# Optimization experiments

Hardware: AMD Instinct MI355X
Metric: run time of the kernel (lower is better)

## Reference

```python
import jax, jax.numpy as jnp
import numpy as np


def setup_inputs() -> dict:
    key = jax.random.key(0)
    k1, k2 = jax.random.split(key)
    B, T, D, N = 8, 1024, 256, 8192
    x = jax.random.normal(k1, (B, T, D), dtype=jnp.float32)
    # codebook (kaiming-uniform in torch; gaussian stand-in, same math downstream)
    embed = jax.random.normal(k2, (N, D), dtype=jnp.float32)
    return {"x": x, "embed": embed}


def reference(x, embed):
    # encode: squared-Euclidean distances (argmin-equivalent to torch.cdist)
    x_sq = jnp.sum(x * x, axis=-1, keepdims=True)          # [B,T,1]
    e_sq = jnp.sum(embed * embed, axis=-1)                 # [N]
    xe = jnp.einsum('btd,nd->btn', x, embed)               # [B,T,N]
    dist2 = x_sq - 2.0 * xe + e_sq                         # [B,T,N]
    embed_ind = jnp.argmin(dist2, axis=-1)                 # [B,T] int
    # decode: embedding gather
    quantized = jnp.take(embed, embed_ind, axis=0)         # [B,T,D]
    return quantized, embed_ind
```

## Files before the change

kernel.cpp:

```cpp
#include <hip/hip_runtime.h>
#include <hip/hip_fp16.h>

typedef __attribute__((ext_vector_type(8))) _Float16 f16x8;
typedef __attribute__((ext_vector_type(16))) float f32x16;

#define M_TOT 8192
#define N_TOT 8192
#define K_TOT 256

__device__ __forceinline__ void load_lds16(const void* g, void* l) {
  __builtin_amdgcn_global_load_lds(
      (const __attribute__((address_space(1))) unsigned int*)g,
      (__attribute__((address_space(3))) unsigned int*)l, 16, 0, 0);
}
__device__ __forceinline__ double shfl_xor_d(double v, int m) {
  unsigned long long u = (unsigned long long)__double_as_longlong(v);
  unsigned lo = (unsigned)u, hi = (unsigned)(u >> 32);
  lo = __shfl_xor(lo, m, 64);
  hi = __shfl_xor(hi, m, 64);
  return __longlong_as_double((long long)((((unsigned long long)hi) << 32) | lo));
}

__global__ __launch_bounds__(256) void prep_kernel(
    const float* __restrict__ x, const float* __restrict__ embed,
    unsigned short* __restrict__ X0p, unsigned short* __restrict__ E0p,
    float* __restrict__ xsq, float* __restrict__ esq) {
  const int bid = blockIdx.x;
  const bool is_e = bid >= 2048;
  const int lb = is_e ? bid - 2048 : bid;
  const int t = lb * 256 + threadIdx.x;
  const float* __restrict__ in = is_e ? embed : x;
  unsigned short* __restrict__ p0 = is_e ? E0p : X0p;
  float* __restrict__ sq = is_e ? esq : xsq;

  float4 v = reinterpret_cast<const float4*>(in)[t];
  float f[4] = {v.x, v.y, v.z, v.w};
  unsigned short h[4];
#pragma unroll
  for (int c = 0; c < 4; ++c) h[c] = __half_as_ushort(__float2half_rn(f[c]));
  ushort4 o = {h[0], h[1], h[2], h[3]};
  reinterpret_cast<ushort4*>(p0)[t] = o;

  const int lane = threadIdx.x & 63;
  float s = f[0] * f[0] + f[1] * f[1] + f[2] * f[2] + f[3] * f[3];
#pragma unroll
  for (int off = 32; off > 0; off >>= 1) s += __shfl_xor(s, off, 64);
  if (lane == 0) sq[lb * 4 + (threadIdx.x >> 6)] = s;
}

__global__ __launch_bounds__(256, 3) void mfma_pmin_kernel(
    const unsigned short* __restrict__ X0p, const unsigned short* __restrict__ E0p,
    const float* __restrict__ esq, unsigned short* __restrict__ pmin) {
  __shared__ unsigned short lds[16384];

  const int tid = threadIdx.x;
  const int wid = tid >> 6;
  const int lane = tid & 63;
  const int li = lane & 15;
  const int lh = (lane >> 4) & 1;
  const int lq2 = lane >> 5;

  const int bid = blockIdx.x;
  const int nb = (bid & 7) * 8 + ((bid >> 3) & 7);
  const int mb = bid >> 6;
  const int m0 = mb * 128, n0 = nb * 128;
  const int wn = (wid >> 1) * 64, wm = (wid & 1) * 64;

  const int r_st = lane >> 2;
  const int kp_st = ((lane & 3) - (r_st >> 1)) & 3;
  const int sw_k0 = (li * 4 + ((lq2 + (li >> 1)) & 3)) * 8;
  const int sw_k1 = (li * 4 + ((2 + lq2 + (li >> 1)) & 3)) * 8;

  f32x16 acc[2][2];
#pragma unroll
  for (int a = 0; a < 2; ++a)
#pragma unroll
    for (int b = 0; b < 2; ++b)
#pragma unroll
      for (int r = 0; r < 16; ++r) acc[a][b][r] = 0.0f;

  const int eseg = (wn >> 4) + lh;
  const int xseg = (wm >> 4) + lh;

  for (int kc = 0; kc < 4; ++kc) {
    const int k0 = kc * 64;
    __syncthreads();
#pragma unroll
    for (int j = 0; j < 8; ++j) {
      const int tt = j * 4 + wid;
      const int tsel = tt >> 4;
      const int u = tt & 15;
      const int ksl = u >> 3, seg = u & 7;
      const int rowbase = (tsel ? m0 : n0) + seg * 16 + r_st;
      const unsigned short* src = tsel ? X0p : E0p;
      load_lds16(src + (size_t)rowbase * K_TOT + k0 + ksl * 32 + kp_st * 8,
                 &lds[tsel * 8192 + ksl * 4096 + seg * 512]);
    }
    __syncthreads();

#pragma unroll
    for (int ksl = 0; ksl < 2; ++ksl) {
      const unsigned short* Eb = &lds[ksl * 4096];
      const unsigned short* Xb = &lds[8192 + ksl * 4096];
      f16x8 ef[2][2];
#pragma unroll
      for (int et = 0; et < 2; ++et) {
        const unsigned short* eb = Eb + (eseg + et * 2) * 512;
        ef[et][0] = *(const f16x8*)(eb + sw_k0);
        ef[et][1] = *(const f16x8*)(eb + sw_k1);
      }
#pragma unroll
      for (int xt = 0; xt < 2; ++xt) {
        const unsigned short* xb = Xb + (xseg + xt * 2) * 512;
        f16x8 xf0 = *(const f16x8*)(xb + sw_k0);
        f16x8 xf1 = *(const f16x8*)(xb + sw_k1);
#pragma unroll
        for (int et = 0; et < 2; ++et) {
          f32x16 c = acc[et][xt];
          c = __builtin_amdgcn_mfma_f32_32x32x16_f16(ef[et][0], xf0, c, 0, 0, 0);
          c = __builtin_amdgcn_mfma_f32_32x32x16_f16(ef[et][1], xf1, c, 0, 0, 0);
          acc[et][xt] = c;
        }
      }
    }
  }

  float es[2][16];
#pragma unroll
  for (int et = 0; et < 2; ++et)
#pragma unroll
    for (int r = 0; r < 16; ++r)
      es[et][r] = esq[n0 + wn + et * 32 + (r & 3) + 8 * (r >> 2) + 4 * lq2];

#pragma unroll
  for (int xt = 0; xt < 2; ++xt) {
    unsigned short outv[4];
#pragma unroll
    for (int et = 0; et < 2; ++et) {
#pragma unroll
      for (int cell = 0; cell < 2; ++cell) {
        float mval = 3.4e38f;
#pragma unroll
        for (int rr = 0; rr < 8; ++rr) {
          const int r = cell * 8 + rr;
          mval = fminf(mval, es[et][r] - 2.0f * acc[et][xt][r]);
        }
        mval = fminf(mval, __shfl_xor(mval, 32, 64));
        outv[et * 2 + cell] = __half_as_ushort(__float2half_rd(mval));
      }
    }
    if (lq2 == 0) {
      const int xrow = m0 + wm + xt * 32 + (lane & 31);
      *reinterpret_cast<ushort4*>(&pmin[(size_t)xrow * 512 + ((n0 + wn) >> 4)]) =
          *reinterpret_cast<ushort4*>(outv);
    }
  }
}

__global__ __launch_bounds__(256) void refine_gather_kernel(
    const float* __restrict__ x, const float* __restrict__ embed,
    const float* __restrict__ xsq, const unsigned short* __restrict__ pmin,
    float* __restrict__ out) {
  const int row = blockIdx.x * 4 + (threadIdx.x >> 6);
  const int lane = threadIdx.x & 63;

  const unsigned short* pm = pmin + (size_t)row * 512 + lane * 8;
  int4 raw = *reinterpret_cast<const int4*>(pm);
  unsigned short cu[8];
  *reinterpret_cast<int4*>(cu) = raw;
  float cv[8];
#pragma unroll
  for (int j = 0; j < 8; ++j) cv[j] = __half2float(__ushort_as_half(cu[j]));
  float lm = cv[0];
#pragma unroll
  for (int j = 1; j < 8; ++j) lm = fminf(lm, cv[j]);
#pragma unroll
  for (int off = 1; off < 64; off <<= 1) lm = fminf(lm, __shfl_xor(lm, off, 64));

  const float thr = lm + sqrtf(xsq[row]) * (96.0f / 1024.0f) + 1.2f;

  const int c = lane & 15, q = lane >> 4;
  const float* xp = x + (size_t)row * K_TOT + q * 64;

  double bd = 1e300;
  int bidx = 1 << 30;
#pragma unroll
  for (int j = 0; j < 8; ++j) {
    unsigned long long mask = __ballot(cv[j] < thr);
    while (mask) {
      const int b = __ffsll((long long)mask) - 1;
      mask &= mask - 1;
      const int cell = b * 8 + j;
      const int col = cell * 16 + c;
      const float* ep = embed + (size_t)col * K_TOT + q * 64;
      double dd = 0.0;
#pragma unroll
      for (int i = 0; i < 16; ++i) {
        float4 e4 = reinterpret_cast<const float4*>(ep)[i];
        float4 x4 = reinterpret_cast<const float4*>(xp)[i];
        double d0 = (double)x4.x - (double)e4.x;
        double d1 = (double)x4.y - (double)e4.y;
        double d2 = (double)x4.z - (double)e4.z;
        double d3 = (double)x4.w - (double)e4.w;
        dd += d0 * d0 + d1 * d1 + d2 * d2 + d3 * d3;
      }
      dd += shfl_xor_d(dd, 16);
      dd += shfl_xor_d(dd, 32);
      int ci = col;
#pragma unroll
      for (int off = 1; off < 16; off <<= 1) {
        double od = shfl_xor_d(dd, off);
        int oi = __shfl_xor(ci, off, 64);
        if (od < dd || (od == dd && oi < ci)) { dd = od; ci = oi; }
      }
      if (dd < bd || (dd == bd && ci < bidx)) { bd = dd; bidx = ci; }
    }
  }

  reinterpret_cast<float4*>(out)[(size_t)row * 64 + lane] =
      reinterpret_cast<const float4*>(embed)[(size_t)bidx * 64 + lane];
  if (lane == 0) out[(size_t)M_TOT * K_TOT + row] = (float)bidx;
}

#define BM 32
#define BN 64
#define KC 32
#define NQ 2
#define NPQ (N_TOT / NQ)
#define SB 72

__global__ __launch_bounds__(256) void esq_kernel(const float* __restrict__ embed,
                                                  float* __restrict__ esq) {
  const int lane = threadIdx.x & 63;
  const int wave = threadIdx.x >> 6;
  const int code = blockIdx.x * 4 + wave;
  float4 v = reinterpret_cast<const float4*>(embed + (size_t)code * K_TOT)[lane];
  float s = v.x * v.x + v.y * v.y + v.z * v.z + v.w * v.w;
#pragma unroll
  for (int off = 32; off > 0; off >>= 1) s += __shfl_xor(s, off, 64);
  if (lane == 0) esq[code] = s;
}

__global__ __launch_bounds__(256, 2) void argmin_kernel(
    const float* __restrict__ x, const float* __restrict__ embed,
    const float* __restrict__ esq, float* __restrict__ pval, int* __restrict__ pidx) {
  __shared__ float A[K_TOT][BM];
  __shared__ float Bs[KC][SB];
  const int tid = threadIdx.x;
  const int tx = tid & 15;
  const int ty = tid >> 4;
  const int q = blockIdx.x & 1;
  const int mb = blockIdx.x >> 1;
  const int m0 = mb * BM;
  const int nq0 = q * NPQ;
#pragma unroll
  for (int it = 0; it < 8; ++it) {
    int idx = it * 256 + tid;
    int row = idx >> 6;
    int k4 = idx & 63;
    float4 v = reinterpret_cast<const float4*>(x + (size_t)(m0 + row) * K_TOT)[k4];
    A[k4 * 4 + 0][row] = v.x; A[k4 * 4 + 1][row] = v.y;
    A[k4 * 4 + 2][row] = v.z; A[k4 * 4 + 3][row] = v.w;
  }
  float minv[2]; int mini[2];
#pragma unroll
  for (int r = 0; r < 2; ++r) { minv[r] = 3.4e38f; mini[r] = 0; }
  for (int ns = 0; ns < NPQ / BN; ++ns) {
    const int n0 = nq0 + ns * BN;
    float acc[2][4];
#pragma unroll
    for (int r = 0; r < 2; ++r)
#pragma unroll
      for (int c = 0; c < 4; ++c) acc[r][c] = 0.0f;
    for (int kc = 0; kc < K_TOT / KC; ++kc) {
      const int k0 = kc * KC;
      __syncthreads();
#pragma unroll
      for (int it = 0; it < 2; ++it) {
        int idx = it * 256 + tid;
        int nl = idx >> 3;
        int k4 = idx & 7;
        float4 v = reinterpret_cast<const float4*>(embed + (size_t)(n0 + nl) * K_TOT + k0)[k4];
        Bs[k4 * 4 + 0][nl] = v.x; Bs[k4 * 4 + 1][nl] = v.y;
        Bs[k4 * 4 + 2][nl] = v.z; Bs[k4 * 4 + 3][nl] = v.w;
      }
      __syncthreads();
#pragma unroll
      for (int kk = 0; kk < KC; ++kk) {
        float2 a = *reinterpret_cast<const float2*>(&A[k0 + kk][ty * 2]);
        float4 b = *reinterpret_cast<const float4*>(&Bs[kk][tx * 4]);
        acc[0][0] += a.x * b.x; acc[0][1] += a.x * b.y;
        acc[0][2] += a.x * b.z; acc[0][3] += a.x * b.w;
        acc[1][0] += a.y * b.x; acc[1][1] += a.y * b.y;
        acc[1][2] += a.y * b.z; acc[1][3] += a.y * b.w;
      }
    }
    float4 es = *reinterpret_cast<const float4*>(&esq[n0 + tx * 4]);
    float e[4] = {es.x, es.y, es.z, es.w};
#pragma unroll
    for (int r = 0; r < 2; ++r)
#pragma unroll
      for (int c = 0; c < 4; ++c) {
        float d = e[c] - 2.0f * acc[r][c];
        int id = n0 + tx * 4 + c;
        if (d < minv[r]) { minv[r] = d; mini[r] = id; }
      }
  }
#pragma unroll
  for (int r = 0; r < 2; ++r) {
    float v = minv[r]; int i = mini[r];
#pragma unroll
    for (int off = 1; off < 16; off <<= 1) {
      float vo = __shfl_xor(v, off, 64);
      int io = __shfl_xor(i, off, 64);
      if (vo < v || (vo == v && io < i)) { v = vo; i = io; }
    }
    if (tx == 0) {
      int row = m0 + ty * 2 + r;
      pval[q * M_TOT + row] = v;
      pidx[q * M_TOT + row] = i;
    }
  }
}

__global__ __launch_bounds__(256) void gather_kernel(
    const float* __restrict__ embed, const float* __restrict__ pval,
    const int* __restrict__ pidx, float* __restrict__ out) {
  const int row = blockIdx.x;
  float bv = pval[row]; int bi = pidx[row];
#pragma unroll
  for (int qq = 1; qq < NQ; ++qq) {
    float v = pval[qq * M_TOT + row];
    int i = pidx[qq * M_TOT + row];
    if (v < bv || (v == bv && i < bi)) { bv = v; bi = i; }
  }
  out[(size_t)row * K_TOT + threadIdx.x] = embed[(size_t)bi * K_TOT + threadIdx.x];
  if (threadIdx.x == 0) out[(size_t)M_TOT * K_TOT + row] = (float)bi;
}

extern "C" void kernel_launch(void* const* d_in, const int* in_sizes, int n_in,
                              void* d_out, int out_size, void* d_ws, size_t ws_size,
                              hipStream_t stream) {
  const float* x = (const float*)d_in[0];
  const float* embed = (const float*)d_in[1];
  float* out = (float*)d_out;
  char* ws = (char*)d_ws;

  const size_t HALF_BYTES = (size_t)M_TOT * K_TOT * 2;
  const size_t PMIN_BYTES = (size_t)M_TOT * 512 * 2;
  const size_t need = (1u << 20) + 2 * HALF_BYTES + PMIN_BYTES;

  if (ws_size >= need) {
    float* xsq = (float*)ws;
    float* esq = (float*)(ws + 32768);
    unsigned short* X0p = (unsigned short*)(ws + (1u << 20));
    unsigned short* E0p = (unsigned short*)(ws + (1u << 20) + HALF_BYTES);
    unsigned short* pmin = (unsigned short*)(ws + (1u << 20) + 2 * HALF_BYTES);
    prep_kernel<<<4096, 256, 0, stream>>>(x, embed, X0p, E0p, xsq, esq);
    mfma_pmin_kernel<<<4096, 256, 0, stream>>>(X0p, E0p, esq, pmin);
    refine_gather_kernel<<<2048, 256, 0, stream>>>(x, embed, xsq, pmin, out);
  } else {
    float* esq = (float*)ws;
    float* pval = (float*)(ws + 32768);
    int* pidx = (int*)(ws + 32768 + NQ * 32768);
    esq_kernel<<<2048, 256, 0, stream>>>(embed, esq);
    argmin_kernel<<<512, 256, 0, stream>>>(x, embed, esq, pval, pidx);
    gather_kernel<<<M_TOT, 256, 0, stream>>>(embed, pval, pidx, out);
  }
}
```

Baseline: 150.6 us.

## Fuse prep, MFMA pmin and refine kernels into one persistent kernel with grid barriers

Merges the three launches into a single persistent kernel of 768 blocks that loops over work items in each phase. The phases are separated by a software grid barrier built on atomics, which removes the launch gaps and tail effects between kernels. The cost is barrier spin overhead and a hipMemsetAsync to reset the counter. It also relies on all 768 blocks being co-resident (3 per CU), and it will deadlock if they are not.

```diff
diff --git a/kernel.cpp b/kernel.cpp
--- a/kernel.cpp
+++ b/kernel.cpp
@@ -7,6 +7,7 @@
 #define M_TOT 8192
 #define N_TOT 8192
 #define K_TOT 256
+#define NBLK 768
 
 __device__ __forceinline__ void load_lds16(const void* g, void* l) {
   __builtin_amdgcn_global_load_lds(
@@ -21,205 +22,215 @@
   return __longlong_as_double((long long)((((unsigned long long)hi) << 32) | lo));
 }
 
-__global__ __launch_bounds__(256) void prep_kernel(
+__device__ __forceinline__ void grid_bar(unsigned* cnt, unsigned* sense, unsigned gen) {
+  __syncthreads();
+  if (threadIdx.x == 0) {
+    __threadfence();
+    unsigned arrived =
+        __hip_atomic_fetch_add(cnt, 1u, __ATOMIC_ACQ_REL, __HIP_MEMORY_SCOPE_AGENT) + 1;
+    if (arrived == gen * NBLK) {
+      __hip_atomic_store(sense, gen, __ATOMIC_RELEASE, __HIP_MEMORY_SCOPE_AGENT);
+    } else {
+      while (__hip_atomic_load(sense, __ATOMIC_ACQUIRE, __HIP_MEMORY_SCOPE_AGENT) < gen) {
+      }
+    }
+    __threadfence();
+  }
+  __syncthreads();
+}
+
+__global__ __launch_bounds__(256, 3) void fused_kernel(
     const float* __restrict__ x, const float* __restrict__ embed,
     unsigned short* __restrict__ X0p, unsigned short* __restrict__ E0p,
-    float* __restrict__ xsq, float* __restrict__ esq) {
-  const int bid = blockIdx.x;
-  const bool is_e = bid >= 2048;
-  const int lb = is_e ? bid - 2048 : bid;
-  const int t = lb * 256 + threadIdx.x;
-  const float* __restrict__ in = is_e ? embed : x;
-  unsigned short* __restrict__ p0 = is_e ? E0p : X0p;
-  float* __restrict__ sq = is_e ? esq : xsq;
-
-  float4 v = reinterpret_cast<const float4*>(in)[t];
-  float f[4] = {v.x, v.y, v.z, v.w};
-  unsigned short h[4];
-#pragma unroll
-  for (int c = 0; c < 4; ++c) h[c] = __half_as_ushort(__float2half_rn(f[c]));
-  ushort4 o = {h[0], h[1], h[2], h[3]};
-  reinterpret_cast<ushort4*>(p0)[t] = o;
-
-  const int lane = threadIdx.x & 63;
-  float s = f[0] * f[0] + f[1] * f[1] + f[2] * f[2] + f[3] * f[3];
-#pragma unroll
-  for (int off = 32; off > 0; off >>= 1) s += __shfl_xor(s, off, 64);
-  if (lane == 0) sq[lb * 4 + (threadIdx.x >> 6)] = s;
-}
-
-__global__ __launch_bounds__(256, 3) void mfma_pmin_kernel(
-    const unsigned short* __restrict__ X0p, const unsigned short* __restrict__ E0p,
-    const float* __restrict__ esq, unsigned short* __restrict__ pmin) {
+    float* __restrict__ xsq, float* __restrict__ esq,
+    unsigned short* __restrict__ pmin, unsigned* __restrict__ bar,
+    float* __restrict__ out) {
   __shared__ unsigned short lds[16384];
 
   const int tid = threadIdx.x;
   const int wid = tid >> 6;
   const int lane = tid & 63;
+
+  for (int rw = blockIdx.x * 4 + wid; rw < 16384; rw += NBLK * 4) {
+    const bool is_e = rw >= 8192;
+    const int row = rw & 8191;
+    const float* __restrict__ in = is_e ? embed : x;
+    unsigned short* __restrict__ p0 = is_e ? E0p : X0p;
+    float4 v = reinterpret_cast<const float4*>(in + (size_t)row * K_TOT)[lane];
+    float f[4] = {v.x, v.y, v.z, v.w};
+    unsigned short h[4];
+#pragma unroll
+    for (int c = 0; c < 4; ++c) h[c] = __half_as_ushort(__float2half_rn(f[c]));
+    ushort4 o = {h[0], h[1], h[2], h[3]};
+    reinterpret_cast<ushort4*>(p0 + (size_t)row * K_TOT)[lane] = o;
+    float s = f[0] * f[0] + f[1] * f[1] + f[2] * f[2] + f[3] * f[3];
+#pragma unroll
+    for (int off = 32; off > 0; off >>= 1) s += __shfl_xor(s, off, 64);
+    if (lane == 0) (is_e ? esq : xsq)[row] = s;
+  }
+
+  grid_bar(bar, bar + 1, 1);
+
   const int li = lane & 15;
   const int lh = (lane >> 4) & 1;
   const int lq2 = lane >> 5;
-
-  const int bid = blockIdx.x;
-  const int nb = (bid & 7) * 8 + ((bid >> 3) & 7);
-  const int mb = bid >> 6;
-  const int m0 = mb * 128, n0 = nb * 128;
-  const int wn = (wid >> 1) * 64, wm = (wid & 1) * 64;
-
   const int r_st = lane >> 2;
   const int kp_st = ((lane & 3) - (r_st >> 1)) & 3;
   const int sw_k0 = (li * 4 + ((lq2 + (li >> 1)) & 3)) * 8;
   const int sw_k1 = (li * 4 + ((2 + lq2 + (li >> 1)) & 3)) * 8;
 
-  f32x16 acc[2][2];
-#pragma unroll
-  for (int a = 0; a < 2; ++a)
-#pragma unroll
-    for (int b = 0; b < 2; ++b)
-#pragma unroll
-      for (int r = 0; r < 16; ++r) acc[a][b][r] = 0.0f;
-
-  const int eseg = (wn >> 4) + lh;
-  const int xseg = (wm >> 4) + lh;
-
-  for (int kc = 0; kc < 4; ++kc) {
-    const int k0 = kc * 64;
-    __syncthreads();
+  for (int t = blockIdx.x; t < 4096; t += NBLK) {
+    const int nb = (t & 7) * 8 + ((t >> 3) & 7);
+    const int mb = t >> 6;
+    const int m0 = mb * 128, n0 = nb * 128;
+    const int wn = (wid >> 1) * 64, wm = (wid & 1) * 64;
+
+    f32x16 acc[2][2];
+#pragma unroll
+    for (int a = 0; a < 2; ++a)
+#pragma unroll
+      for (int b = 0; b < 2; ++b)
+#pragma unroll
+        for (int r = 0; r < 16; ++r) acc[a][b][r] = 0.0f;
+
+    const int eseg = (wn >> 4) + lh;
+    const int xseg = (wm >> 4) + lh;
+
+    for (int kc = 0; kc < 4; ++kc) {
+      const int k0 = kc * 64;
+      __syncthreads();
+#pragma unroll
+      for (int j = 0; j < 8; ++j) {
+        const int tt = j * 4 + wid;
+        const int tsel = tt >> 4;
+        const int u = tt & 15;
+        const int ksl = u >> 3, seg = u & 7;
+        const int rowbase = (tsel ? m0 : n0) + seg * 16 + r_st;
+        const unsigned short* src = tsel ? X0p : E0p;
+        load_lds16(src + (size_t)rowbase * K_TOT + k0 + ksl * 32 + kp_st * 8,
+                   &lds[tsel * 8192 + ksl * 4096 + seg * 512]);
+      }
+      __syncthreads();
+
+#pragma unroll
+      for (int ksl = 0; ksl < 2; ++ksl) {
+        const unsigned short* Eb = &lds[ksl * 4096];
+        const unsigned short* Xb = &lds[8192 + ksl * 4096];
+        f16x8 ef[2][2];
+#pragma unroll
+        for (int et = 0; et < 2; ++et) {
+          const unsigned short* eb = Eb + (eseg + et * 2) * 512;
+          ef[et][0] = *(const f16x8*)(eb + sw_k0);
+          ef[et][1] = *(const f16x8*)(eb + sw_k1);
+        }
+#pragma unroll
+        for (int xt = 0; xt < 2; ++xt) {
+          const unsigned short* xb = Xb + (xseg + xt * 2) * 512;
+          f16x8 xf0 = *(const f16x8*)(xb + sw_k0);
+          f16x8 xf1 = *(const f16x8*)(xb + sw_k1);
+#pragma unroll
+          for (int et = 0; et < 2; ++et) {
+            f32x16 c = acc[et][xt];
+            c = __builtin_amdgcn_mfma_f32_32x32x16_f16(ef[et][0], xf0, c, 0, 0, 0);
+            c = __builtin_amdgcn_mfma_f32_32x32x16_f16(ef[et][1], xf1, c, 0, 0, 0);
+            acc[et][xt] = c;
+          }
+        }
+      }
+    }
+
+    float es[2][16];
+#pragma unroll
+    for (int et = 0; et < 2; ++et)
+#pragma unroll
+      for (int r = 0; r < 16; ++r)
+        es[et][r] = esq[n0 + wn + et * 32 + (r & 3) + 8 * (r >> 2) + 4 * lq2];
+
+#pragma unroll
+    for (int xt = 0; xt < 2; ++xt) {
+      unsigned short outv[4];
+#pragma unroll
+      for (int et = 0; et < 2; ++et) {
+#pragma unroll
+        for (int cell = 0; cell < 2; ++cell) {
+          float mval = 3.4e38f;
+#pragma unroll
+          for (int rr = 0; rr < 8; ++rr) {
+            const int r = cell * 8 + rr;
+            mval = fminf(mval, es[et][r] - 2.0f * acc[et][xt][r]);
+          }
+          mval = fminf(mval, __shfl_xor(mval, 32, 64));
+          outv[et * 2 + cell] = __half_as_ushort(__float2half_rd(mval));
+        }
+      }
+      if (lq2 == 0) {
+        const int xrow = m0 + wm + xt * 32 + (lane & 31);
+        *reinterpret_cast<ushort4*>(&pmin[(size_t)xrow * 512 + ((n0 + wn) >> 4)]) =
+            *reinterpret_cast<ushort4*>(outv);
+      }
+    }
+  }
+
+  grid_bar(bar, bar + 1, 2);
+
+  for (int row = blockIdx.x * 4 + wid; row < 8192; row += NBLK * 4) {
+    const unsigned short* pm = pmin + (size_t)row * 512 + lane * 8;
+    int4 raw = *reinterpret_cast<const int4*>(pm);
+    unsigned short cu[8];
+    *reinterpret_cast<int4*>(cu) = raw;
+    float cv[8];
+#pragma unroll
+    for (int j = 0; j < 8; ++j) cv[j] = __half2float(__ushort_as_half(cu[j]));
+    float lm = cv[0];
+#pragma unroll
+    for (int j = 1; j < 8; ++j) lm = fminf(lm, cv[j]);
+#pragma unroll
+    for (int off = 1; off < 64; off <<= 1) lm = fminf(lm, __shfl_xor(lm, off, 64));
+
+    const float thr = lm + sqrtf(xsq[row]) * (96.0f / 1024.0f) + 1.2f;
+
+    const int c = lane & 15, q = lane >> 4;
+    const float* xp = x + (size_t)row * K_TOT + q * 64;
+
+    double bd = 1e300;
+    int bidx = 1 << 30;
 #pragma unroll
     for (int j = 0; j < 8; ++j) {
-      const int tt = j * 4 + wid;
-      const int tsel = tt >> 4;
-      const int u = tt & 15;
-      const int ksl = u >> 3, seg = u & 7;
-      const int rowbase = (tsel ? m0 : n0) + seg * 16 + r_st;
-      const unsigned short* src = tsel ? X0p : E0p;
-      load_lds16(src + (size_t)rowbase * K_TOT + k0 + ksl * 32 + kp_st * 8,
-                 &lds[tsel * 8192 + ksl * 4096 + seg * 512]);
-    }
-    __syncthreads();
-
-#pragma unroll
-    for (int ksl = 0; ksl < 2; ++ksl) {
-      const unsigned short* Eb = &lds[ksl * 4096];
-      const unsigned short* Xb = &lds[8192 + ksl * 4096];
-      f16x8 ef[2][2];
-#pragma unroll
-      for (int et = 0; et < 2; ++et) {
-        const unsigned short* eb = Eb + (eseg + et * 2) * 512;
-        ef[et][0] = *(const f16x8*)(eb + sw_k0);
-        ef[et][1] = *(const f16x8*)(eb + sw_k1);
-      }
-#pragma unroll
-      for (int xt = 0; xt < 2; ++xt) {
-        const unsigned short* xb = Xb + (xseg + xt * 2) * 512;
-        f16x8 xf0 = *(const f16x8*)(xb + sw_k0);
-        f16x8 xf1 = *(const f16x8*)(xb + sw_k1);
-#pragma unroll
-        for (int et = 0; et < 2; ++et) {
-          f32x16 c = acc[et][xt];
-          c = __builtin_amdgcn_mfma_f32_32x32x16_f16(ef[et][0], xf0, c, 0, 0, 0);
-          c = __builtin_amdgcn_mfma_f32_32x32x16_f16(ef[et][1], xf1, c, 0, 0, 0);
-          acc[et][xt] = c;
-        }
-      }
-    }
-  }
-
-  float es[2][16];
-#pragma unroll
-  for (int et = 0; et < 2; ++et)
-#pragma unroll
-    for (int r = 0; r < 16; ++r)
-      es[et][r] = esq[n0 + wn + et * 32 + (r & 3) + 8 * (r >> 2) + 4 * lq2];
-
-#pragma unroll
-  for (int xt = 0; xt < 2; ++xt) {
-    unsigned short outv[4];
-#pragma unroll
-    for (int et = 0; et < 2; ++et) {
-#pragma unroll
-      for (int cell = 0; cell < 2; ++cell) {
-        float mval = 3.4e38f;
-#pragma unroll
-        for (int rr = 0; rr < 8; ++rr) {
-          const int r = cell * 8 + rr;
-          mval = fminf(mval, es[et][r] - 2.0f * acc[et][xt][r]);
-        }
-        mval = fminf(mval, __shfl_xor(mval, 32, 64));
-        outv[et * 2 + cell] = __half_as_ushort(__float2half_rd(mval));
-      }
-    }
-    if (lq2 == 0) {
-      const int xrow = m0 + wm + xt * 32 + (lane & 31);
-      *reinterpret_cast<ushort4*>(&pmin[(size_t)xrow * 512 + ((n0 + wn) >> 4)]) =
-          *reinterpret_cast<ushort4*>(outv);
-    }
-  }
-}
-
-__global__ __launch_bounds__(256) void refine_gather_kernel(
-    const float* __restrict__ x, const float* __restrict__ embed,
-    const float* __restrict__ xsq, const unsigned short* __restrict__ pmin,
-    float* __restrict__ out) {
-  const int row = blockIdx.x * 4 + (threadIdx.x >> 6);
-  const int lane = threadIdx.x & 63;
-
-  const unsigned short* pm = pmin + (size_t)row * 512 + lane * 8;
-  int4 raw = *reinterpret_cast<const int4*>(pm);
-  unsigned short cu[8];
-  *reinterpret_cast<int4*>(cu) = raw;
-  float cv[8];
-#pragma unroll
-  for (int j = 0; j < 8; ++j) cv[j] = __half2float(__ushort_as_half(cu[j]));
-  float lm = cv[0];
-#pragma unroll
-  for (int j = 1; j < 8; ++j) lm = fminf(lm, cv[j]);
-#pragma unroll
-  for (int off = 1; off < 64; off <<= 1) lm = fminf(lm, __shfl_xor(lm, off, 64));
-
-  const float thr = lm + sqrtf(xsq[row]) * (96.0f / 1024.0f) + 1.2f;
-
-  const int c = lane & 15, q = lane >> 4;
-  const float* xp = x + (size_t)row * K_TOT + q * 64;
-
-  double bd = 1e300;
-  int bidx = 1 << 30;
-#pragma unroll
-  for (int j = 0; j < 8; ++j) {
-    unsigned long long mask = __ballot(cv[j] < thr);
-    while (mask) {
-      const int b = __ffsll((long long)mask) - 1;
-      mask &= mask - 1;
-      const int cell = b * 8 + j;
-      const int col = cell * 16 + c;
-      const float* ep = embed + (size_t)col * K_TOT + q * 64;
-      double dd = 0.0;
-#pragma unroll
-      for (int i = 0; i < 16; ++i) {
-        float4 e4 = reinterpret_cast<const float4*>(ep)[i];
-        float4 x4 = reinterpret_cast<const float4*>(xp)[i];
-        double d0 = (double)x4.x - (double)e4.x;
-        double d1 = (double)x4.y - (double)e4.y;
-        double d2 = (double)x4.z - (double)e4.z;
-        double d3 = (double)x4.w - (double)e4.w;
-        dd += d0 * d0 + d1 * d1 + d2 * d2 + d3 * d3;
-      }
-      dd += shfl_xor_d(dd, 16);
-      dd += shfl_xor_d(dd, 32);
-      int ci = col;
-#pragma unroll
-      for (int off = 1; off < 16; off <<= 1) {
-        double od = shfl_xor_d(dd, off);
-        int oi = __shfl_xor(ci, off, 64);
-        if (od < dd || (od == dd && oi < ci)) { dd = od; ci = oi; }
-      }
-      if (dd < bd || (dd == bd && ci < bidx)) { bd = dd; bidx = ci; }
-    }
-  }
-
-  reinterpret_cast<float4*>(out)[(size_t)row * 64 + lane] =
-      reinterpret_cast<const float4*>(embed)[(size_t)bidx * 64 + lane];
-  if (lane == 0) out[(size_t)M_TOT * K_TOT + row] = (float)bidx;
+      unsigned long long mask = __ballot(cv[j] < thr);
+      while (mask) {
+        const int b = __ffsll((long long)mask) - 1;
+        mask &= mask - 1;
+        const int cell = b * 8 + j;
+        const int col = cell * 16 + c;
+        const float* ep = embed + (size_t)col * K_TOT + q * 64;
+        double dd = 0.0;
+#pragma unroll
+        for (int i = 0; i < 16; ++i) {
+          float4 e4 = reinterpret_cast<const float4*>(ep)[i];
+          float4 x4 = reinterpret_cast<const float4*>(xp)[i];
+          double d0 = (double)x4.x - (double)e4.x;
+          double d1 = (double)x4.y - (double)e4.y;
+          double d2 = (double)x4.z - (double)e4.z;
+          double d3 = (double)x4.w - (double)e4.w;
+          dd += d0 * d0 + d1 * d1 + d2 * d2 + d3 * d3;
+        }
+        dd += shfl_xor_d(dd, 16);
+        dd += shfl_xor_d(dd, 32);
+        int ci = col;
+#pragma unroll
+        for (int off = 1; off < 16; off <<= 1) {
+          double od = shfl_xor_d(dd, off);
+          int oi = __shfl_xor(ci, off, 64);
+          if (od < dd || (od == dd && oi < ci)) { dd = od; ci = oi; }
+        }
+        if (dd < bd || (dd == bd && ci < bidx)) { bd = dd; bidx = ci; }
+      }
+    }
+
+    reinterpret_cast<float4*>(out)[(size_t)row * 64 + lane] =
+        reinterpret_cast<const float4*>(embed)[(size_t)bidx * 64 + lane];
+    if (lane == 0) out[(size_t)M_TOT * K_TOT + row] = (float)bidx;
+  }
 }
 
 #define BM 32
@@ -351,14 +362,14 @@
   const size_t need = (1u << 20) + 2 * HALF_BYTES + PMIN_BYTES;
 
   if (ws_size >= need) {
-    float* xsq = (float*)ws;
-    float* esq = (float*)(ws + 32768);
+    unsigned* bar = (unsigned*)ws;
+    float* xsq = (float*)(ws + 65536);
+    float* esq = (float*)(ws + 65536 + 32768);
     unsigned short* X0p = (unsigned short*)(ws + (1u << 20));
     unsigned short* E0p = (unsigned short*)(ws + (1u << 20) + HALF_BYTES);
     unsigned short* pmin = (unsigned short*)(ws + (1u << 20) + 2 * HALF_BYTES);
-    prep_kernel<<<4096, 256, 0, stream>>>(x, embed, X0p, E0p, xsq, esq);
-    mfma_pmin_kernel<<<4096, 256, 0, stream>>>(X0p, E0p, esq, pmin);
-    refine_gather_kernel<<<2048, 256, 0, stream>>>(x, embed, xsq, pmin, out);
+    hipMemsetAsync(bar, 0, 64, stream);
+    fused_kernel<<<NBLK, 256, 0, stream>>>(x, embed, X0p, E0p, xsq, esq, pmin, bar, out);
   } else {
     float* esq = (float*)ws;
     float* pval = (float*)(ws + 32768);
```

Result: slower. 392.5 us (+160.6%).
